# Kernel optimization log

Hardware: AMD Instinct MI355X
Metric: run time of the kernel (lower is better)

Reference implementation:

```python
import jax, jax.numpy as jnp
import numpy as np

EPS = 1e-7          # K.epsilon()
START_TEMP = 10.0
MIN_TEMP = 0.1
ALPHA = 0.99999


def setup_inputs() -> dict:
    key = jax.random.key(0)
    k1, k2, k3, k4 = jax.random.split(key, 4)
    batch, n_feat, bins, out_dim = 4096, 20000, 64, 256
    X = jax.random.normal(k1, (batch, n_feat), dtype=jnp.float32)
    u = jax.random.normal(k2, (n_feat, bins), dtype=jnp.float32)
    # keras 'uniform' initializer ~ U(-0.05, 0.05)
    tinyW = jax.random.uniform(k3, (bins, out_dim), minval=-0.05, maxval=0.05, dtype=jnp.float32)
    uniform = jax.random.uniform(k4, (out_dim, n_feat), minval=EPS, maxval=1.0, dtype=jnp.float32)
    return {"X": X, "u": u, "tinyW": tinyW, "uniform": uniform}


def reference(X, u, tinyW, uniform):
    # al = softmax(u @ tinyW) over output_dim axis, then transpose -> (D, N)
    al = jax.nn.softmax(jnp.dot(u, tinyW), axis=-1).T            # (D, N)
    logits = jnp.log(10.0 * jnp.clip(al, EPS, 0.9999999))        # (D, N)
    gumbel = -jnp.log(-jnp.log(uniform))                          # (D, N)
    temp = jnp.maximum(MIN_TEMP, START_TEMP * ALPHA)              # one K.update step
    samples = jax.nn.softmax((logits + gumbel) / temp, axis=-1)   # (D, N)

    D, N = samples.shape

    # Greedy global-argmax with row/column suppression (inference path).
    # Each of the D iterations picks the global max of p, marks dl[x, y] = 1,
    # then masks row x and column y with -1 (as the numpy loop does).
    def step(carry, _):
        p, dl = carry
        ind = jnp.argmax(p)            # flat argmax over D*N
        x = ind // N
        y = ind % N
        dl = dl.at[x, y].set(1.0)
        p = p.at[x, :].set(-1.0)
        p = p.at[:, y].set(-1.0)
        return (p, dl), None

    (_, dl), _ = jax.lax.scan(step, (samples, jnp.zeros_like(samples)), None, length=D)
    # After D iterations each row of dl has exactly one 1, so
    # one_hot(argmax(dl, axis=-1)) == dl; selections = dl in inference mode.
    Y = jnp.dot(X, dl.T)               # (batch, D)
    return Y
```

## Files before the change

kernel.cpp:

```cpp
#include <hip/hip_runtime.h>
#include <cmath>
#include <cfloat>
#include <climits>

#define NFEAT 20000
#define DDIM 256
#define KDIM 64
#define SEGN 32
#define NSEG 625
#define SEGP 640

#define LOG2E 1.4426950408889634
#define INVT (1.0 / 9.9999)
#define LOG2_10 3.3219280948873623
#define G2C 0.5287663729448976
#define LO2 -23.253496664211536
#define HI2 -1.4426951130237154e-7

__device__ __forceinline__ double fexp2(double x) {
  const double nd = rint(x);
  const double y = (x - nd) * 0.6931471805599453;
  double p = 1.0 / 3628800.0;
  p = fma(p, y, 1.0 / 362880.0);
  p = fma(p, y, 1.0 / 40320.0);
  p = fma(p, y, 1.0 / 5040.0);
  p = fma(p, y, 1.0 / 720.0);
  p = fma(p, y, 1.0 / 120.0);
  p = fma(p, y, 1.0 / 24.0);
  p = fma(p, y, 1.0 / 6.0);
  p = fma(p, y, 0.5);
  p = fma(p, y, 1.0);
  p = fma(p, y, 1.0);
  const int n = (int)nd;
  const double sc = __longlong_as_double((long long)(n + 1023) << 52);
  return p * sc;
}

__device__ __forceinline__ double flog2(double x) {
  const long long b = __double_as_longlong(x);
  int e = (int)(b >> 52) - 1023;
  double m = __longlong_as_double((b & 0xfffffffffffffLL) | 0x3ff0000000000000LL);
  if (m > 1.4142135623730951) { m *= 0.5; e += 1; }
  const double t = (m - 1.0) / (m + 1.0);
  const double w = t * t;
  double p = 1.0 / 13.0;
  p = fma(p, w, 1.0 / 11.0);
  p = fma(p, w, 1.0 / 9.0);
  p = fma(p, w, 1.0 / 7.0);
  p = fma(p, w, 1.0 / 5.0);
  p = fma(p, w, 1.0 / 3.0);
  p = fma(p, w, 1.0);
  return fma((2.0 * LOG2E) * t, p, (double)e);
}

__device__ __forceinline__ double z2_post(double L2raw, float uu) {
  const double L2 = fmin(fmax(L2raw, LO2), HI2);
  const double t = -flog2((double)uu);
  const double g2 = G2C - flog2(t);
  return (LOG2_10 + L2 + g2) * INVT;
}

__device__ __forceinline__ double compute_z2(
    const float* __restrict__ u, const float* __restrict__ W,
    const float* __restrict__ unif, const double* __restrict__ lseN,
    int dd, int n) {
  double acc = 0.0;
  const float* ur = u + (size_t)n * KDIM;
#pragma unroll 8
  for (int k = 0; k < KDIM; ++k)
    acc = fma((double)ur[k] * LOG2E, (double)W[k * DDIM + dd], acc);
  return z2_post(acc - lseN[n], unif[(size_t)dd * NFEAT + n]);
}

__global__ __launch_bounds__(256) void k_seg(
    const float* __restrict__ u, const float* __restrict__ W,
    const float* __restrict__ unif, double* __restrict__ lseN,
    double* __restrict__ segVal, double* __restrict__ segSum,
    int* __restrict__ segCol) {
  const int s = blockIdx.x;
  const int n0 = s * SEGN;
  const int d = threadIdx.x;
  const int lane = d & 63, w = d >> 6;

  __shared__ __align__(16) double ut2[SEGN][KDIM];
  __shared__ float unT[SEGN][DDIM];
  __shared__ double ssum[4][8];
  __shared__ double lse2s[8];

  for (int i = d; i < SEGN * KDIM; i += 256)
    ut2[i >> 6][i & 63] =
        (double)u[(size_t)(n0 + (i >> 6)) * KDIM + (i & 63)] * LOG2E;
  for (int q = 0; q < SEGN; q += 4) {
    const float4 t = *(const float4*)(unif + (size_t)d * NFEAT + n0 + q);
    unT[q + 0][d] = t.x;
    unT[q + 1][d] = t.y;
    unT[q + 2][d] = t.z;
    unT[q + 3][d] = t.w;
  }
  float wcol[KDIM];
#pragma unroll
  for (int k = 0; k < KDIM; ++k) wcol[k] = W[k * DDIM + d];
  __syncthreads();

  double ssl = 0.0;
  double segm = -INFINITY;
  int segc = -1;

  for (int b0 = 0; b0 < SEGN; b0 += 8) {
    double acc[8];
#pragma unroll
    for (int i = 0; i < 8; ++i) acc[i] = 0.0;
#pragma unroll
    for (int k4 = 0; k4 < 16; ++k4) {
      const int kb = k4 * 4;
      const double w0 = (double)wcol[kb + 0], w1 = (double)wcol[kb + 1];
      const double w2 = (double)wcol[kb + 2], w3 = (double)wcol[kb + 3];
#pragma unroll
      for (int i = 0; i < 8; ++i) {
        const double2 ua = *(const double2*)&ut2[b0 + i][kb];
        const double2 ub = *(const double2*)&ut2[b0 + i][kb + 2];
        acc[i] = fma(ua.x, w0, acc[i]);
        acc[i] = fma(ua.y, w1, acc[i]);
        acc[i] = fma(ub.x, w2, acc[i]);
        acc[i] = fma(ub.y, w3, acc[i]);
      }
    }
    double sl[8];
#pragma unroll
    for (int i = 0; i < 8; ++i) sl[i] = fexp2(acc[i]);
#pragma unroll
    for (int off = 1; off < 64; off <<= 1)
#pragma unroll
      for (int i = 0; i < 8; ++i) sl[i] += __shfl_xor(sl[i], off, 64);
    if (lane == 0)
#pragma unroll
      for (int i = 0; i < 8; ++i) ssum[w][i] = sl[i];
    __syncthreads();
    if (d < 8) {
      const double tot = ssum[0][d] + ssum[1][d] + ssum[2][d] + ssum[3][d];
      const double lz = flog2(tot);
      lse2s[d] = lz;
      lseN[n0 + b0 + d] = lz;
    }
    __syncthreads();
#pragma unroll 2
    for (int i = 0; i < 8; ++i) {
      const double z2 = z2_post(acc[i] - lse2s[i], unT[b0 + i][d]);
      ssl += fexp2(z2);
      if (z2 > segm) { segm = z2; segc = n0 + b0 + i; }
    }
    __syncthreads();
  }
  segVal[(size_t)d * SEGP + s] = segm;
  segCol[(size_t)d * SEGP + s] = segc;
  segSum[(size_t)d * SEGP + s] = ssl;
}

__global__ __launch_bounds__(64) void k_rowstat(
    const double* __restrict__ segVal, const double* __restrict__ segSum,
    const int* __restrict__ segCol, double* __restrict__ logL,
    double* __restrict__ bestKey, int* __restrict__ bestCol) {
  const int dd = blockIdx.x, lane = threadIdx.x;
  double sum = 0.0, bv = -INFINITY;
  int bc = INT_MAX;
  for (int s = lane; s < NSEG; s += 64) {
    sum += segSum[(size_t)dd * SEGP + s];
    double v = segVal[(size_t)dd * SEGP + s];
    int c = segCol[(size_t)dd * SEGP + s];
    if (c >= 0 && (v > bv || (v == bv && c < bc))) { bv = v; bc = c; }
  }
#pragma unroll
  for (int off = 32; off > 0; off >>= 1) {
    sum += __shfl_xor(sum, off, 64);
    double ov = __shfl_xor(bv, off, 64);
    int oc = __shfl_xor(bc, off, 64);
    if (ov > bv || (ov == bv && oc < bc)) { bv = ov; bc = oc; }
  }
  if (lane == 0) {
    double lL = flog2(sum);
    logL[dd] = lL;
    bestKey[dd] = bv - lL;
    bestCol[dd] = bc;
  }
}

__global__ __launch_bounds__(64) void k_greedy(
    const float* __restrict__ u, const float* __restrict__ W,
    const float* __restrict__ unif, const double* __restrict__ lseN,
    double* __restrict__ segVal, int* __restrict__ segCol,
    const double* __restrict__ logL, const double* __restrict__ bestKey,
    const int* __restrict__ bestCol, int* __restrict__ sel) {
  const int lane = threadIdx.x;
  __shared__ double kk[DDIM], sk[DDIM];
  __shared__ int sr[DDIM], sc[DDIM], selL[DDIM];
  __shared__ unsigned int supp[NFEAT / 32];
  for (int i = lane; i < NFEAT / 32; i += 64) supp[i] = 0u;

  double myk[4];
  int myc[4];
#pragma unroll
  for (int i = 0; i < 4; ++i) {
    int dd = lane + 64 * i;
    myk[i] = bestKey[dd];
    myc[i] = bestCol[dd];
    kk[dd] = myk[i];
  }
  __syncthreads();
#pragma unroll
  for (int i = 0; i < 4; ++i) {
    int dd = lane + 64 * i;
    int rk = 0;
#pragma unroll 4
    for (int j = 0; j < DDIM; ++j) {
      double kj = kk[j];
      if (kj > myk[i] || (kj == myk[i] && j < dd)) ++rk;
    }
    sk[rk] = myk[i];
    sr[rk] = dd;
    sc[rk] = myc[i];
  }
  __syncthreads();

  int pos = 0;
  for (int guard = 0; guard < 4 * DDIM && pos < DDIM; ++guard) {
    const int p = pos + lane;
    const bool valid = p < DDIM;
    int r = -1, c = -1000000 - lane;
    if (valid) { r = sr[p]; c = sc[p]; }
    bool conf = !valid;
    if (valid) conf = (supp[c >> 5] >> (c & 31)) & 1u;
    bool dup = false;
#pragma unroll
    for (int j = 0; j < 63; ++j) {
      int cj = __shfl(c, j, 64);
      if (j < lane && cj == c) dup = true;
    }
    if (valid && dup) conf = true;
    unsigned long long bm = __ballot(conf);
    int fc = bm ? (__ffsll(bm) - 1) : 64;
    if (lane < fc) {
      selL[r] = c;
      atomicOr(&supp[c >> 5], 1u << (c & 31));
    }
    __syncthreads();
    pos += fc;
    if (fc < 64 && pos < DDIM) {
      const int rr = sr[pos];
      double pbv = -INFINITY;
      int pbc = INT_MAX;
      int stale[10];
      int scnt = 0;
#pragma unroll
      for (int i2 = 0; i2 < 10; ++i2) {
        int s2 = lane + 64 * i2;
        if (s2 < NSEG) {
          double v = segVal[(size_t)rr * SEGP + s2];
          int cc = segCol[(size_t)rr * SEGP + s2];
          if (cc >= 0) {
            if ((supp[cc >> 5] >> (cc & 31)) & 1u) stale[scnt++] = s2;
            else if (v > pbv || (v == pbv && cc < pbc)) { pbv = v; pbc = cc; }
          }
        }
      }
      unsigned long long sm2 = __ballot(scnt > 0);
      for (int g2 = 0; g2 < NSEG + 4 && sm2; ++g2) {
        int src = __ffsll(sm2) - 1;
        int cand = (scnt > 0) ? stale[scnt - 1] : 0;
        int s2 = __shfl(cand, src, 64);
        if (lane == src) --scnt;
        int ccol = s2 * SEGN + lane;
        double zv = -INFINITY;
        if (lane < SEGN && !((supp[ccol >> 5] >> (ccol & 31)) & 1u))
          zv = compute_z2(u, W, unif, lseN, rr, ccol);
        int zc = (zv == -INFINITY) ? INT_MAX : ccol;
#pragma unroll
        for (int off = 32; off > 0; off >>= 1) {
          double ov = __shfl_xor(zv, off, 64);
          int oc = __shfl_xor(zc, off, 64);
          if (ov > zv || (ov == zv && oc < zc)) { zv = ov; zc = oc; }
        }
        if (lane == 0) {
          segVal[(size_t)rr * SEGP + s2] = (zc == INT_MAX) ? -INFINITY : zv;
          segCol[(size_t)rr * SEGP + s2] = (zc == INT_MAX) ? -1 : zc;
        }
        if (zc != INT_MAX && (zv > pbv || (zv == pbv && zc < pbc))) {
          pbv = zv;
          pbc = zc;
        }
        sm2 = __ballot(scnt > 0);
      }
#pragma unroll
      for (int off = 32; off > 0; off >>= 1) {
        double ov = __shfl_xor(pbv, off, 64);
        int oc = __shfl_xor(pbc, off, 64);
        if (ov > pbv || (ov == pbv && oc < pbc)) { pbv = ov; pbc = oc; }
      }
      const double knew = pbv - logL[rr];
      const int cn = pbc;
      int cnt = 0;
      for (int q = pos + 1 + lane; q < DDIM; q += 64) {
        double kq = sk[q];
        int rq = sr[q];
        if (kq > knew || (kq == knew && rq < rr)) ++cnt;
      }
#pragma unroll
      for (int off = 32; off > 0; off >>= 1) cnt += __shfl_xor(cnt, off, 64);
      for (int q0 = pos + 1; q0 <= pos + cnt; q0 += 64) {
        int q = q0 + lane;
        double tk = 0.0;
        int tr = 0, tc = 0;
        bool v2 = q <= pos + cnt;
        if (v2) { tk = sk[q]; tr = sr[q]; tc = sc[q]; }
        __syncthreads();
        if (v2) { sk[q - 1] = tk; sr[q - 1] = tr; sc[q - 1] = tc; }
        __syncthreads();
      }
      if (lane == 0) { sk[pos + cnt] = knew; sr[pos + cnt] = rr; sc[pos + cnt] = cn; }
      __syncthreads();
    }
  }
#pragma unroll
  for (int i = 0; i < 4; ++i) sel[lane + 64 * i] = selL[lane + 64 * i];
}

__global__ __launch_bounds__(256) void k_gather(const float* __restrict__ X,
                                                float* out) {
  const int dd = threadIdx.x;
  const size_t b = (size_t)blockIdx.x + 1;
  const int y = __float_as_int(out[dd]);
  out[b * DDIM + dd] = X[b * NFEAT + y];
}

__global__ __launch_bounds__(256) void k_row0(const float* __restrict__ X,
                                              float* out) {
  const int dd = threadIdx.x;
  const int y = __float_as_int(out[dd]);
  const float v = X[y];
  out[dd] = v;
}

extern "C" void kernel_launch(void* const* d_in, const int* in_sizes, int n_in,
                              void* d_out, int out_size, void* d_ws,
                              size_t ws_size, hipStream_t stream) {
  (void)in_sizes; (void)n_in; (void)d_ws; (void)ws_size; (void)out_size;
  const float* X = (const float*)d_in[0];
  const float* u = (const float*)d_in[1];
  const float* W = (const float*)d_in[2];
  const float* unif = (const float*)d_in[3];

  char* ob = (char*)d_out;
  int* sel = (int*)ob;
  double* lseN = (double*)(ob + 1024);
  double* logL = (double*)(ob + 161024);
  double* bestKey = (double*)(ob + 163072);
  int* bestCol = (int*)(ob + 165120);
  double* segVal = (double*)(ob + 166144);
  double* segSum = (double*)(ob + 1476864);
  int* segCol = (int*)(ob + 2787584);

  k_seg<<<NSEG, 256, 0, stream>>>(u, W, unif, lseN, segVal, segSum, segCol);
  k_rowstat<<<DDIM, 64, 0, stream>>>(segVal, segSum, segCol, logL, bestKey,
                                     bestCol);
  k_greedy<<<1, 64, 0, stream>>>(u, W, unif, lseN, segVal, segCol, logL,
                                 bestKey, bestCol, sel);
  k_gather<<<4095, 256, 0, stream>>>(X, (float*)d_out);
  k_row0<<<1, 256, 0, stream>>>(X, (float*)d_out);
}
```

Baseline: 633.7 us.

## Fold row statistics into segment kernel via atomics and fast reciprocal in log2

Removes the k_rowstat kernel. k_seg now atomically accumulates per-row softmax sums and a packed max key (value bits plus inverted column) into a small buffer, and k_greedy derives logL and the best key itself. Replaces the double division in flog2 with v_rcp_f64 plus two Newton steps. When a workspace is available it gathers all rows in one kernel instead of the gather and row0 pair. Truncating the key's low 16 bits can change ties among near-equal maxima, and the float atomic sums are non-deterministic.

```diff
diff --git a/kernel.cpp b/kernel.cpp
--- a/kernel.cpp
+++ b/kernel.cpp
@@ -16,6 +16,14 @@
 #define G2C 0.5287663729448976
 #define LO2 -23.253496664211536
 #define HI2 -1.4426951130237154e-7
+
+__device__ __forceinline__ double frcp(double a) {
+  double r;
+  asm("v_rcp_f64 %0, %1" : "=v"(r) : "v"(a));
+  r = fma(fma(-a, r, 1.0), r, r);
+  r = fma(fma(-a, r, 1.0), r, r);
+  return r;
+}
 
 __device__ __forceinline__ double fexp2(double x) {
   const double nd = rint(x);
@@ -41,7 +49,7 @@
   int e = (int)(b >> 52) - 1023;
   double m = __longlong_as_double((b & 0xfffffffffffffLL) | 0x3ff0000000000000LL);
   if (m > 1.4142135623730951) { m *= 0.5; e += 1; }
-  const double t = (m - 1.0) / (m + 1.0);
+  const double t = (m - 1.0) * frcp(m + 1.0);
   const double w = t * t;
   double p = 1.0 / 13.0;
   p = fma(p, w, 1.0 / 11.0);
@@ -72,11 +80,23 @@
   return z2_post(acc - lseN[n], unif[(size_t)dd * NFEAT + n]);
 }
 
+__device__ __forceinline__ unsigned long long dkey(double v) {
+  const long long b = __double_as_longlong(v);
+  const unsigned long long ub = (unsigned long long)b;
+  return (b < 0) ? ~ub : (ub | 0x8000000000000000ull);
+}
+
+__global__ __launch_bounds__(256) void k_init(double* __restrict__ rowSum,
+                                              unsigned long long* __restrict__ rowKey) {
+  rowSum[threadIdx.x] = 0.0;
+  rowKey[threadIdx.x] = 0ull;
+}
+
 __global__ __launch_bounds__(256) void k_seg(
     const float* __restrict__ u, const float* __restrict__ W,
     const float* __restrict__ unif, double* __restrict__ lseN,
-    double* __restrict__ segVal, double* __restrict__ segSum,
-    int* __restrict__ segCol) {
+    double* __restrict__ segVal, int* __restrict__ segCol,
+    double* __restrict__ rowSum, unsigned long long* __restrict__ rowKey) {
   const int s = blockIdx.x;
   const int n0 = s * SEGN;
   const int d = threadIdx.x;
@@ -153,45 +173,20 @@
   }
   segVal[(size_t)d * SEGP + s] = segm;
   segCol[(size_t)d * SEGP + s] = segc;
-  segSum[(size_t)d * SEGP + s] = ssl;
-}
-
-__global__ __launch_bounds__(64) void k_rowstat(
-    const double* __restrict__ segVal, const double* __restrict__ segSum,
-    const int* __restrict__ segCol, double* __restrict__ logL,
-    double* __restrict__ bestKey, int* __restrict__ bestCol) {
-  const int dd = blockIdx.x, lane = threadIdx.x;
-  double sum = 0.0, bv = -INFINITY;
-  int bc = INT_MAX;
-  for (int s = lane; s < NSEG; s += 64) {
-    sum += segSum[(size_t)dd * SEGP + s];
-    double v = segVal[(size_t)dd * SEGP + s];
-    int c = segCol[(size_t)dd * SEGP + s];
-    if (c >= 0 && (v > bv || (v == bv && c < bc))) { bv = v; bc = c; }
-  }
-#pragma unroll
-  for (int off = 32; off > 0; off >>= 1) {
-    sum += __shfl_xor(sum, off, 64);
-    double ov = __shfl_xor(bv, off, 64);
-    int oc = __shfl_xor(bc, off, 64);
-    if (ov > bv || (ov == bv && oc < bc)) { bv = ov; bc = oc; }
-  }
-  if (lane == 0) {
-    double lL = flog2(sum);
-    logL[dd] = lL;
-    bestKey[dd] = bv - lL;
-    bestCol[dd] = bc;
-  }
+  atomicAdd(&rowSum[d], ssl);
+  atomicMax(&rowKey[d], (dkey(segm) & 0xFFFFFFFFFFFF0000ull) |
+                            (unsigned long long)(0xFFFF - segc));
 }
 
 __global__ __launch_bounds__(64) void k_greedy(
     const float* __restrict__ u, const float* __restrict__ W,
     const float* __restrict__ unif, const double* __restrict__ lseN,
     double* __restrict__ segVal, int* __restrict__ segCol,
-    const double* __restrict__ logL, const double* __restrict__ bestKey,
-    const int* __restrict__ bestCol, int* __restrict__ sel) {
+    const double* __restrict__ rowSum,
+    const unsigned long long* __restrict__ rowKey, int* __restrict__ sel,
+    int* __restrict__ selWs) {
   const int lane = threadIdx.x;
-  __shared__ double kk[DDIM], sk[DDIM];
+  __shared__ double kk[DDIM], sk[DDIM], logLs[DDIM];
   __shared__ int sr[DDIM], sc[DDIM], selL[DDIM];
   __shared__ unsigned int supp[NFEAT / 32];
   for (int i = lane; i < NFEAT / 32; i += 64) supp[i] = 0u;
@@ -200,9 +195,14 @@
   int myc[4];
 #pragma unroll
   for (int i = 0; i < 4; ++i) {
-    int dd = lane + 64 * i;
-    myk[i] = bestKey[dd];
-    myc[i] = bestCol[dd];
+    const int dd = lane + 64 * i;
+    const double lL = flog2(rowSum[dd]);
+    logLs[dd] = lL;
+    const unsigned long long key = rowKey[dd];
+    const int col = 0xFFFF - (int)(key & 0xFFFFull);
+    const double bv = segVal[(size_t)dd * SEGP + (col >> 5)];
+    myk[i] = bv - lL;
+    myc[i] = col;
     kk[dd] = myk[i];
   }
   __syncthreads();
@@ -295,7 +295,7 @@
         int oc = __shfl_xor(pbc, off, 64);
         if (ov > pbv || (ov == pbv && oc < pbc)) { pbv = ov; pbc = oc; }
       }
-      const double knew = pbv - logL[rr];
+      const double knew = pbv - logLs[rr];
       const int cn = pbc;
       int cnt = 0;
       for (int q = pos + 1 + lane; q < DDIM; q += 64) {
@@ -320,7 +320,18 @@
     }
   }
 #pragma unroll
-  for (int i = 0; i < 4; ++i) sel[lane + 64 * i] = selL[lane + 64 * i];
+  for (int i = 0; i < 4; ++i) {
+    const int v = selL[lane + 64 * i];
+    sel[lane + 64 * i] = v;
+    if (selWs) selWs[lane + 64 * i] = v;
+  }
+}
+
+__global__ __launch_bounds__(256) void k_gather_all(
+    const float* __restrict__ X, const int* __restrict__ selWs, float* out) {
+  const int dd = threadIdx.x;
+  const size_t b = (size_t)blockIdx.x;
+  out[b * DDIM + dd] = X[b * NFEAT + selWs[dd]];
 }
 
 __global__ __launch_bounds__(256) void k_gather(const float* __restrict__ X,
@@ -342,7 +353,7 @@
 extern "C" void kernel_launch(void* const* d_in, const int* in_sizes, int n_in,
                               void* d_out, int out_size, void* d_ws,
                               size_t ws_size, hipStream_t stream) {
-  (void)in_sizes; (void)n_in; (void)d_ws; (void)ws_size; (void)out_size;
+  (void)in_sizes; (void)n_in; (void)out_size;
   const float* X = (const float*)d_in[0];
   const float* u = (const float*)d_in[1];
   const float* W = (const float*)d_in[2];
@@ -351,18 +362,23 @@
   char* ob = (char*)d_out;
   int* sel = (int*)ob;
   double* lseN = (double*)(ob + 1024);
-  double* logL = (double*)(ob + 161024);
-  double* bestKey = (double*)(ob + 163072);
-  int* bestCol = (int*)(ob + 165120);
-  double* segVal = (double*)(ob + 166144);
-  double* segSum = (double*)(ob + 1476864);
-  int* segCol = (int*)(ob + 2787584);
-
-  k_seg<<<NSEG, 256, 0, stream>>>(u, W, unif, lseN, segVal, segSum, segCol);
-  k_rowstat<<<DDIM, 64, 0, stream>>>(segVal, segSum, segCol, logL, bestKey,
-                                     bestCol);
-  k_greedy<<<1, 64, 0, stream>>>(u, W, unif, lseN, segVal, segCol, logL,
-                                 bestKey, bestCol, sel);
-  k_gather<<<4095, 256, 0, stream>>>(X, (float*)d_out);
-  k_row0<<<1, 256, 0, stream>>>(X, (float*)d_out);
-}
+  double* rowSum = (double*)(ob + 161024);
+  unsigned long long* rowKey = (unsigned long long*)(ob + 163072);
+  double* segVal = (double*)(ob + 165120);
+  int* segCol = (int*)(ob + 1475840);
+
+  const bool use_ws = (d_ws != nullptr) && (ws_size >= 4096);
+  int* selWs = use_ws ? (int*)d_ws : nullptr;
+
+  k_init<<<1, 256, 0, stream>>>(rowSum, rowKey);
+  k_seg<<<NSEG, 256, 0, stream>>>(u, W, unif, lseN, segVal, segCol, rowSum,
+                                  rowKey);
+  k_greedy<<<1, 64, 0, stream>>>(u, W, unif, lseN, segVal, segCol, rowSum,
+                                 rowKey, sel, selWs);
+  if (use_ws) {
+    k_gather_all<<<4096, 256, 0, stream>>>(X, selWs, (float*)d_out);
+  } else {
+    k_gather<<<4095, 256, 0, stream>>>(X, (float*)d_out);
+    k_row0<<<1, 256, 0, stream>>>(X, (float*)d_out);
+  }
+}
```

After: 623.2 us. About the same (-1.7%).
